# Performance work log

Hardware: AMD Instinct MI355X
Metric: run time of the kernel (lower is better)

Reference implementation:

```python
import jax, jax.numpy as jnp
import numpy as np

N, E, DIN, DH, ED, H, C = 50000, 800000, 384, 256, 32, 4, 64
EPS = 1e-5


def setup_inputs() -> dict:
    key = jax.random.key(0)
    ks = jax.random.split(key, 32)
    w = lambda k, shape, fan: (jax.random.normal(k, shape, jnp.float32) / np.float32(np.sqrt(fan)))
    inp = {
        'x': jax.random.normal(ks[0], (N, DIN), jnp.float32),
        'edge_index': jax.random.randint(ks[1], (2, E), 0, N, dtype=jnp.int32),
        'edge_attr': jax.random.normal(ks[2], (E, ED), jnp.float32),
        'W_in': w(ks[3], (DIN, DH), DIN), 'b_in': jnp.zeros((DH,), jnp.float32),
        'W_out': w(ks[4], (DH, DH), DH), 'b_out': jnp.zeros((DH,), jnp.float32),
    }
    for i in range(2):
        o = 5 + 6 * i
        inp[f'Wl{i}'] = w(ks[o + 0], (DH, H * C), DH)
        inp[f'bl{i}'] = jnp.zeros((H * C,), jnp.float32)
        inp[f'Wr{i}'] = w(ks[o + 1], (DH, H * C), DH)
        inp[f'br{i}'] = jnp.zeros((H * C,), jnp.float32)
        inp[f'We{i}'] = w(ks[o + 2], (ED, H * C), ED)
        inp[f'att{i}'] = w(ks[o + 3], (H, C), C)
        inp[f'bias{i}'] = jnp.zeros((H * C,), jnp.float32)
        inp[f'g{i}'] = jnp.ones((DH,), jnp.float32)
        inp[f'beta{i}'] = jnp.zeros((DH,), jnp.float32)
    return inp


def _gatv2(h, src, dst, ea, Wl, bl, Wr, br, We, att, bias):
    # h: [N, DH]; src/dst: [Etot]; ea: [Etot, ED]
    xl = (h @ Wl + bl).reshape(N, H, C)
    xr = (h @ Wr + br).reshape(N, H, C)
    ee = (ea @ We).reshape(-1, H, C)
    m = jax.nn.leaky_relu(xl[src] + xr[dst] + ee, 0.2)  # [Etot,H,C]
    logits = jnp.einsum('ehc,hc->eh', m, att)           # [Etot,H]
    mx = jax.ops.segment_max(logits, dst, num_segments=N)
    p = jnp.exp(logits - mx[dst])
    den = jax.ops.segment_sum(p, dst, num_segments=N)
    alpha = p / den[dst]                                # softmax per dst node
    out = jax.ops.segment_sum(xl[src] * alpha[:, :, None], dst, num_segments=N)
    return out.reshape(N, H * C) + bias


def _graph_norm(h, g, beta):
    # PyG LayerNorm(mode='graph'), batch=None: normalize over all nodes & channels
    mu = h.mean()
    hc = h - mu
    var = (hc * hc).mean()
    return hc / jnp.sqrt(var + EPS) * g + beta


def reference(x, edge_index, edge_attr, W_in, b_in,
              Wl0, bl0, Wr0, br0, We0, att0, bias0, g0, beta0,
              Wl1, bl1, Wr1, br1, We1, att1, bias1, g1, beta1,
              W_out, b_out):
    loops = jnp.arange(N, dtype=edge_index.dtype)
    src = jnp.concatenate([edge_index[0], loops])
    dst = jnp.concatenate([edge_index[1], loops])
    # self-loop edge_attr filled with mean edge feature (PyG fill_value='mean')
    ea = jnp.concatenate([edge_attr, jnp.broadcast_to(edge_attr.mean(0), (N, ED))], axis=0)
    h = jax.nn.relu(x @ W_in + b_in)
    layers = ((Wl0, bl0, Wr0, br0, We0, att0, bias0, g0, beta0),
              (Wl1, bl1, Wr1, br1, We1, att1, bias1, g1, beta1))
    for Wl, bl, Wr, br, We, att, bias, g, beta in layers:
        hn = jax.nn.elu(_gatv2(h, src, dst, ea, Wl, bl, Wr, br, We, att, bias))
        h = _graph_norm(h + hn, g, beta)
    return h @ W_out + b_out
```

## Files before the change

### kernel.cpp

```cpp
#include <hip/hip_runtime.h>
#include <hip/hip_bf16.h>

#define N_NODES 50000
#define E_EDGES 800000
#define DIN_K   384
#define DH_N    256
#define EPSN    1e-5f

typedef unsigned short ushortT;
typedef __attribute__((ext_vector_type(4))) float f32x4;
typedef __attribute__((ext_vector_type(8))) short bf16x8;

static __device__ __forceinline__ float bf2f(unsigned short u)
{
    return __uint_as_float(((unsigned)u) << 16);
}
static __device__ __forceinline__ unsigned short f2bf(float f)
{
    unsigned u = __float_as_uint(f);
    unsigned r = (u + 0x7fffu + ((u >> 16) & 1u)) >> 16;
    return (unsigned short)r;
}
static __device__ __forceinline__ unsigned pack2(float a, float b)
{
    return (unsigned)f2bf(a) | ((unsigned)f2bf(b) << 16);
}

__global__ __launch_bounds__(256) void ea_accum_kernel(const float* __restrict__ ea,
                                                       float* __restrict__ accum, long total)
{
    long stride = (long)gridDim.x * blockDim.x;
    float local = 0.f;
    for (long i = (long)blockIdx.x * blockDim.x + threadIdx.x; i < total; i += stride)
        local += ea[i];
    __shared__ float red[256];
    red[threadIdx.x] = local;
    __syncthreads();
    if (threadIdx.x < 32) {
        float s = 0.f;
#pragma unroll
        for (int r = 0; r < 8; ++r) s += red[r * 32 + threadIdx.x];
        atomicAdd(&accum[threadIdx.x], s);
    }
}

__global__ void hist_kernel(const int* __restrict__ dst, int* __restrict__ counts, int E)
{
    int stride = gridDim.x * blockDim.x;
    for (int e = blockIdx.x * blockDim.x + threadIdx.x; e < E; e += stride)
        atomicAdd(&counts[dst[e]], 1);
}

__global__ __launch_bounds__(1024) void scan_kernel(const int* __restrict__ counts,
                                                    int* __restrict__ offsets, int Nn)
{
    __shared__ int sdata[1024];
    __shared__ int run_s;
    int tid = threadIdx.x;
    if (tid == 0) run_s = 0;
    __syncthreads();
    for (int base2 = 0; base2 < Nn; base2 += 1024) {
        int i = base2 + tid;
        int v = (i < Nn) ? counts[i] : 0;
        sdata[tid] = v;
        __syncthreads();
        for (int off = 1; off < 1024; off <<= 1) {
            int t = (tid >= off) ? sdata[tid - off] : 0;
            __syncthreads();
            sdata[tid] += t;
            __syncthreads();
        }
        int run = run_s;
        if (i < Nn) offsets[i] = run + sdata[tid] - v;
        int tot = sdata[1023];
        __syncthreads();
        if (tid == 0) run_s = run + tot;
        __syncthreads();
    }
    if (tid == 0) offsets[Nn] = run_s;
}

__global__ void scatter_kernel(const int* __restrict__ src, const int* __restrict__ dst,
                               const int* __restrict__ offsets, int* __restrict__ cursors,
                               int* __restrict__ s_src, int* __restrict__ s_dst,
                               int* __restrict__ s_eid, int E)
{
    int stride = gridDim.x * blockDim.x;
    for (int e = blockIdx.x * blockDim.x + threadIdx.x; e < E; e += stride) {
        int d = dst[e];
        int p = offsets[d] + atomicAdd(&cursors[d], 1);
        s_src[p] = src[e];
        s_dst[p] = d;
        s_eid[p] = e;
    }
}

__global__ void eemean_kernel(const float* __restrict__ accum,
                              const float* __restrict__ We0, const float* __restrict__ We1,
                              float* __restrict__ eemean, float invE)
{
    int tid = threadIdx.x;
    int layer = tid >> 8, c = tid & 255;
    const float* W = layer ? We1 : We0;
    float s = 0.f;
#pragma unroll
    for (int j = 0; j < 32; ++j) s += accum[j] * invE * W[j * 256 + c];
    eemean[layer * 256 + c] = s;
}

__global__ __launch_bounds__(256) void transpose_bf16_kernel(const float* __restrict__ in,
                                                             ushortT* __restrict__ out,
                                                             int K, int N)
{
    __shared__ float tile[32][33];
    int bx = blockIdx.x * 32;
    int by = blockIdx.y * 32;
    int tx = threadIdx.x & 31, ty = threadIdx.x >> 5;
#pragma unroll
    for (int r = 0; r < 32; r += 8) {
        int k = by + ty + r, n = bx + tx;
        if (k < K && n < N) tile[ty + r][tx] = in[(size_t)k * N + n];
    }
    __syncthreads();
#pragma unroll
    for (int r = 0; r < 32; r += 8) {
        int n = bx + ty + r, k = by + tx;
        if (n < N && k < K) out[(size_t)n * K + k] = f2bf(tile[tx][ty + r]);
    }
}

__global__ void fuse_bias_kernel(const float* __restrict__ bl, const float* __restrict__ br,
                                 float* __restrict__ out)
{
    int i = threadIdx.x;
    out[i] = (i < 256) ? bl[i] : br[i - 256];
}

__global__ __launch_bounds__(256) void mfma_gemm_kernel(
    const float* __restrict__ A, const ushortT* __restrict__ Bt,
    const float* __restrict__ bias, float* __restrict__ Cf,
    ushortT* __restrict__ Cb, int K, int Nn, int act)
{
    __shared__ __align__(16) ushortT As[128 * 32];
    __shared__ __align__(16) ushortT Bs[128 * 32];
    int tid = threadIdx.x;
    int brow = blockIdx.x * 128;
    int bcol = blockIdx.y * 128;
    int lane = tid & 63, w = tid >> 6;
    int wr = w >> 1, wc = w & 1;
    int fr = lane & 15, fq = lane >> 4;

    f32x4 acc[4][4];
#pragma unroll
    for (int i = 0; i < 4; ++i)
#pragma unroll
        for (int j = 0; j < 4; ++j)
            acc[i][j] = (f32x4){0.f, 0.f, 0.f, 0.f};

    int r0 = tid >> 2, g0 = tid & 3;
    int r1 = r0 + 64;
    int arow0 = brow + r0, arow1 = brow + r1;
    bool av0 = arow0 < N_NODES, av1 = arow1 < N_NODES;
    const float* Ap0 = A + (size_t)arow0 * K + g0 * 8;
    const float* Ap1 = A + (size_t)arow1 * K + g0 * 8;
    const ushortT* Bp0 = Bt + (size_t)(bcol + r0) * K + g0 * 8;
    const ushortT* Bp1 = Bt + (size_t)(bcol + r1) * K + g0 * 8;
    uint4* asw0 = (uint4*)&As[(size_t)tid * 8];
    uint4* asw1 = (uint4*)&As[(size_t)(tid + 256) * 8];
    uint4* bsw0 = (uint4*)&Bs[(size_t)tid * 8];
    uint4* bsw1 = (uint4*)&Bs[(size_t)(tid + 256) * 8];

    for (int k0 = 0; k0 < K; k0 += 32) {
        float4 z = make_float4(0.f, 0.f, 0.f, 0.f);
        float4 fa0 = z, fa1 = z, fc0 = z, fc1 = z;
        if (av0) { fa0 = *(const float4*)(Ap0 + k0); fc0 = *(const float4*)(Ap0 + k0 + 4); }
        if (av1) { fa1 = *(const float4*)(Ap1 + k0); fc1 = *(const float4*)(Ap1 + k0 + 4); }
        uint4 ub0 = *(const uint4*)(Bp0 + k0);
        uint4 ub1 = *(const uint4*)(Bp1 + k0);
        uint4 ua0, ua1;
        ua0.x = pack2(fa0.x, fa0.y); ua0.y = pack2(fa0.z, fa0.w);
        ua0.z = pack2(fc0.x, fc0.y); ua0.w = pack2(fc0.z, fc0.w);
        ua1.x = pack2(fa1.x, fa1.y); ua1.y = pack2(fa1.z, fa1.w);
        ua1.z = pack2(fc1.x, fc1.y); ua1.w = pack2(fc1.z, fc1.w);
        __syncthreads();
        *asw0 = ua0; *asw1 = ua1;
        *bsw0 = ub0; *bsw1 = ub1;
        __syncthreads();

        bf16x8 af[4], bfv[4];
#pragma unroll
        for (int mi = 0; mi < 4; ++mi)
            af[mi] = *(bf16x8*)&As[(size_t)(wr * 64 + mi * 16 + fr) * 32 + fq * 8];
#pragma unroll
        for (int ni = 0; ni < 4; ++ni)
            bfv[ni] = *(bf16x8*)&Bs[(size_t)(wc * 64 + ni * 16 + fr) * 32 + fq * 8];
#pragma unroll
        for (int mi = 0; mi < 4; ++mi)
#pragma unroll
            for (int ni = 0; ni < 4; ++ni)
                acc[mi][ni] = __builtin_amdgcn_mfma_f32_16x16x32_bf16(
                    af[mi], bfv[ni], acc[mi][ni], 0, 0, 0);
    }

#pragma unroll
    for (int ni = 0; ni < 4; ++ni) {
        int col = bcol + wc * 64 + ni * 16 + fr;
        float bv = bias[col];
#pragma unroll
        for (int mi = 0; mi < 4; ++mi) {
#pragma unroll
            for (int r = 0; r < 4; ++r) {
                int row = brow + wr * 64 + mi * 16 + fq * 4 + r;
                if (row < N_NODES) {
                    float t = acc[mi][ni][r] + bv;
                    if (act == 1) t = t > 0.f ? t : 0.f;
                    if (Cf) Cf[(size_t)row * Nn + col] = t;
                    if (Cb) Cb[(size_t)row * Nn + col] = f2bf(t);
                }
            }
        }
    }
}

__global__ __launch_bounds__(256) void edge_logits_kernel(
    const float* __restrict__ ea, const int* __restrict__ s_eid,
    const int* __restrict__ s_src, const int* __restrict__ s_dst,
    const ushortT* __restrict__ Wet, const float* __restrict__ att,
    const ushortT* __restrict__ xlr, float* __restrict__ logits)
{
    __shared__ __align__(16) ushortT Wet_lds[256 * 40];
    __shared__ float att_lds[256];
    __shared__ int sidx[64], didx[64], eidv[64];
    int tid = threadIdx.x;
    int brow = blockIdx.x * 64;

#pragma unroll
    for (int t = 0; t < 4; ++t) {
        int f = tid + t * 256;
        int row = f >> 2, q = f & 3;
        *(uint4*)&Wet_lds[row * 40 + q * 8] = *(const uint4*)(Wet + (size_t)row * 32 + q * 8);
    }
    att_lds[tid] = att[tid];
    if (tid < 64) {
        sidx[tid] = s_src[brow + tid];
        didx[tid] = s_dst[brow + tid];
        eidv[tid] = s_eid[brow + tid];
    }
    __syncthreads();

    int lane = tid & 63, w = tid >> 6;
    int fr = lane & 15, fq = lane >> 4;
    int e_lane = w * 16 + fr;

    int eid = eidv[e_lane];
    const float* earow = ea + (size_t)eid * 32 + fq * 8;
    float4 f0 = ((const float4*)earow)[0];
    float4 f1 = ((const float4*)earow)[1];
    union { unsigned u[4]; bf16x8 v; } ub;
    ub.u[0] = pack2(f0.x, f0.y);
    ub.u[1] = pack2(f0.z, f0.w);
    ub.u[2] = pack2(f1.x, f1.y);
    ub.u[3] = pack2(f1.z, f1.w);
    bf16x8 bfrag = ub.v;

    f32x4 acc[16];
#pragma unroll
    for (int mi = 0; mi < 16; ++mi) {
        bf16x8 afrag = *(bf16x8*)&Wet_lds[(mi * 16 + fr) * 40 + fq * 8];
        acc[mi] = __builtin_amdgcn_mfma_f32_16x16x32_bf16(
            afrag, bfrag, (f32x4){0.f, 0.f, 0.f, 0.f}, 0, 0, 0);
    }

    int sn = sidx[e_lane], dn = didx[e_lane];
    const ushortT* lxp = xlr + (size_t)sn * 512;
    const ushortT* rxp = xlr + (size_t)dn * 512 + 256;
    float part[4] = {0.f, 0.f, 0.f, 0.f};
#pragma unroll
    for (int mi = 0; mi < 16; ++mi) {
        int ch = mi * 16 + fq * 4;
        ushort4 lx = *(const ushort4*)(lxp + ch);
        ushort4 rx = *(const ushort4*)(rxp + ch);
        float4 at = *(const float4*)&att_lds[ch];
        float t0 = acc[mi][0] + bf2f(lx.x) + bf2f(rx.x); t0 = t0 > 0.f ? t0 : 0.2f * t0;
        float t1 = acc[mi][1] + bf2f(lx.y) + bf2f(rx.y); t1 = t1 > 0.f ? t1 : 0.2f * t1;
        float t2 = acc[mi][2] + bf2f(lx.z) + bf2f(rx.z); t2 = t2 > 0.f ? t2 : 0.2f * t2;
        float t3 = acc[mi][3] + bf2f(lx.w) + bf2f(rx.w); t3 = t3 > 0.f ? t3 : 0.2f * t3;
        part[mi >> 2] += t0 * at.x + t1 * at.y + t2 * at.z + t3 * at.w;
    }
#pragma unroll
    for (int hh = 0; hh < 4; ++hh) {
        part[hh] += __shfl_xor(part[hh], 16);
        part[hh] += __shfl_xor(part[hh], 32);
    }
    if (fq == 0) {
        float4 o = make_float4(part[0], part[1], part[2], part[3]);
        *(float4*)&logits[(size_t)(brow + e_lane) * 4] = o;
    }
}

__global__ __launch_bounds__(256) void edge_attn_kernel(
    const int* __restrict__ s_src, const int* __restrict__ offsets,
    const float* __restrict__ logits,
    const float* __restrict__ att, const float* __restrict__ bias,
    const float* __restrict__ eemean,
    const ushortT* __restrict__ xlr, float* __restrict__ h)
{
    int lane = threadIdx.x & 63;
    int d = blockIdx.x * 4 + (threadIdx.x >> 6);
    size_t xbase = (size_t)d * 512 + lane * 4;
    size_t hbase = (size_t)d * 256 + lane * 4;
    int head = lane >> 4;

    ushort4 xlu = *(const ushort4*)(xlr + xbase);
    ushort4 xru = *(const ushort4*)(xlr + xbase + 256);
    float xr0 = bf2f(xru.x), xr1 = bf2f(xru.y), xr2 = bf2f(xru.z), xr3 = bf2f(xru.w);
    float xs0 = bf2f(xlu.x), xs1 = bf2f(xlu.y), xs2 = bf2f(xlu.z), xs3 = bf2f(xlu.w);
    float4 eem = *(const float4*)(eemean + lane * 4);
    float4 at4 = *(const float4*)(att + lane * 4);

    float m = -1e30f, s = 0.f;
    float acc0 = 0.f, acc1 = 0.f, acc2 = 0.f, acc3 = 0.f;
    int beg = offsets[d], end = offsets[d + 1];

    int idx1 = 0;
    ushort4 x_cur = make_ushort4(0, 0, 0, 0);
    float lg_cur = 0.f;
    if (beg < end) {
        int idx0 = s_src[beg];
        x_cur = *(const ushort4*)(xlr + (size_t)idx0 * 512 + lane * 4);
        lg_cur = logits[(size_t)beg * 4 + head];
        if (beg + 1 < end) idx1 = s_src[beg + 1];
    }

    for (int pos = beg; pos < end; ++pos) {
        ushort4 xv = x_cur;
        float lg = lg_cur;
        int np = pos + 1;
        if (np < end) {
            x_cur = *(const ushort4*)(xlr + (size_t)idx1 * 512 + lane * 4);
            lg_cur = logits[(size_t)np * 4 + head];
        }
        if (pos + 2 < end) idx1 = s_src[pos + 2];

        float nm = fmaxf(m, lg);
        float sc = __expf(m - nm);
        float pr = __expf(lg - nm);
        float v0 = bf2f(xv.x), v1 = bf2f(xv.y), v2 = bf2f(xv.z), v3 = bf2f(xv.w);
        s = s * sc + pr;
        acc0 = acc0 * sc + pr * v0;
        acc1 = acc1 * sc + pr * v1;
        acc2 = acc2 * sc + pr * v2;
        acc3 = acc3 * sc + pr * v3;
        m = nm;
    }

    {
        float t0 = xs0 + xr0 + eem.x; t0 = t0 > 0.f ? t0 : 0.2f * t0;
        float t1 = xs1 + xr1 + eem.y; t1 = t1 > 0.f ? t1 : 0.2f * t1;
        float t2 = xs2 + xr2 + eem.z; t2 = t2 > 0.f ? t2 : 0.2f * t2;
        float t3 = xs3 + xr3 + eem.w; t3 = t3 > 0.f ? t3 : 0.2f * t3;
        float lg = t0 * at4.x + t1 * at4.y + t2 * at4.z + t3 * at4.w;
        lg += __shfl_xor(lg, 1);
        lg += __shfl_xor(lg, 2);
        lg += __shfl_xor(lg, 4);
        lg += __shfl_xor(lg, 8);
        float nm = fmaxf(m, lg);
        float sc = __expf(m - nm);
        float pr = __expf(lg - nm);
        s = s * sc + pr;
        acc0 = acc0 * sc + pr * xs0;
        acc1 = acc1 * sc + pr * xs1;
        acc2 = acc2 * sc + pr * xs2;
        acc3 = acc3 * sc + pr * xs3;
    }

    float inv = 1.f / s;
    float4 b4 = *(const float4*)(bias + lane * 4);
    float4 hv = *(const float4*)(h + hbase);
    float o0 = acc0 * inv + b4.x; o0 = o0 > 0.f ? o0 : __expf(o0) - 1.f;
    float o1 = acc1 * inv + b4.y; o1 = o1 > 0.f ? o1 : __expf(o1) - 1.f;
    float o2 = acc2 * inv + b4.z; o2 = o2 > 0.f ? o2 : __expf(o2) - 1.f;
    float o3 = acc3 * inv + b4.w; o3 = o3 > 0.f ? o3 : __expf(o3) - 1.f;
    *(float4*)(h + hbase) = make_float4(hv.x + o0, hv.y + o1, hv.z + o2, hv.w + o3);
}

__global__ __launch_bounds__(256) void stats_kernel(const float* __restrict__ h,
                                                    float* __restrict__ stats)
{
    int stride = gridDim.x * blockDim.x;
    int total = N_NODES * 64;
    float ls = 0.f, lq = 0.f;
    for (int i = blockIdx.x * blockDim.x + threadIdx.x; i < total; i += stride) {
        float4 v = ((const float4*)h)[i];
        ls += v.x + v.y + v.z + v.w;
        lq += v.x * v.x + v.y * v.y + v.z * v.z + v.w * v.w;
    }
#pragma unroll
    for (int o = 1; o < 64; o <<= 1) {
        ls += __shfl_xor(ls, o);
        lq += __shfl_xor(lq, o);
    }
    __shared__ float red[8];
    int lane = threadIdx.x & 63, w = threadIdx.x >> 6;
    if (lane == 0) { red[w * 2] = ls; red[w * 2 + 1] = lq; }
    __syncthreads();
    if (threadIdx.x == 0) {
        atomicAdd(&stats[0], red[0] + red[2] + red[4] + red[6]);
        atomicAdd(&stats[1], red[1] + red[3] + red[5] + red[7]);
    }
}

__global__ void norm_finalize_kernel(float* __restrict__ stats)
{
    float invM = 1.f / ((float)N_NODES * 256.f);
    float mu = stats[0] * invM;
    float var = stats[1] * invM - mu * mu;
    stats[2] = mu;
    stats[3] = rsqrtf(var + EPSN);
}

__global__ void normalize_kernel(float* __restrict__ h, const float* __restrict__ g,
                                 const float* __restrict__ beta, const float* __restrict__ stats)
{
    float mu = stats[2], sc = stats[3];
    int stride = gridDim.x * blockDim.x;
    int total = N_NODES * 64;
    for (int i = blockIdx.x * blockDim.x + threadIdx.x; i < total; i += stride) {
        float4 v = ((float4*)h)[i];
        int k = (i & 63) * 4;
        float4 gv = *(const float4*)&g[k];
        float4 bv = *(const float4*)&beta[k];
        v.x = (v.x - mu) * sc * gv.x + bv.x;
        v.y = (v.y - mu) * sc * gv.y + bv.y;
        v.z = (v.z - mu) * sc * gv.z + bv.z;
        v.w = (v.w - mu) * sc * gv.w + bv.w;
        ((float4*)h)[i] = v;
    }
}

extern "C" void kernel_launch(void* const* d_in, const int* in_sizes, int n_in,
                              void* d_out, int out_size, void* d_ws, size_t ws_size,
                              hipStream_t stream)
{
    (void)in_sizes; (void)n_in; (void)out_size; (void)ws_size;
    const float* x     = (const float*)d_in[0];
    const int*   eidx  = (const int*)d_in[1];
    const float* ea    = (const float*)d_in[2];
    const float* W_in  = (const float*)d_in[3];
    const float* b_in  = (const float*)d_in[4];
    const float* W_out = (const float*)d_in[5];
    const float* b_out = (const float*)d_in[6];
    const float* Wl[2]  = {(const float*)d_in[7],  (const float*)d_in[16]};
    const float* bl[2]  = {(const float*)d_in[8],  (const float*)d_in[17]};
    const float* Wr[2]  = {(const float*)d_in[9],  (const float*)d_in[18]};
    const float* br[2]  = {(const float*)d_in[10], (const float*)d_in[19]};
    const float* We[2]  = {(const float*)d_in[11], (const float*)d_in[20]};
    const float* att[2] = {(const float*)d_in[12], (const float*)d_in[21]};
    const float* bias[2]= {(const float*)d_in[13], (const float*)d_in[22]};
    const float* g[2]   = {(const float*)d_in[14], (const float*)d_in[23]};
    const float* beta[2]= {(const float*)d_in[15], (const float*)d_in[24]};

    char* p = (char*)d_ws;
    auto take = [&](size_t bytes) -> char* {
        char* r = p;
        p += (bytes + 255) & ~(size_t)255;
        return r;
    };
    int*   counts  = (int*)take((size_t)N_NODES * 4);
    int*   cursors = (int*)take((size_t)N_NODES * 4);
    float* ea_acc  = (float*)take(32 * 4);
    float* stats   = (float*)take(8 * 4);
    size_t zero_bytes = (size_t)(p - (char*)d_ws);
    int*   offsets = (int*)take((size_t)(N_NODES + 1) * 4);
    int*   s_src   = (int*)take((size_t)E_EDGES * 4);
    int*   s_dst   = (int*)take((size_t)E_EDGES * 4);
    int*   s_eid   = (int*)take((size_t)E_EDGES * 4);
    float* eemean  = (float*)take(512 * 4);
    ushortT* WtIn  = (ushortT*)take((size_t)256 * 384 * 2);
    ushortT* WtLR0 = (ushortT*)take((size_t)512 * 256 * 2);
    ushortT* WtLR1 = (ushortT*)take((size_t)512 * 256 * 2);
    ushortT* WtOut = (ushortT*)take((size_t)256 * 256 * 2);
    ushortT* Wet0  = (ushortT*)take((size_t)256 * 32 * 2);
    ushortT* Wet1  = (ushortT*)take((size_t)256 * 32 * 2);
    float* fb0     = (float*)take(512 * 4);
    float* fb1     = (float*)take(512 * 4);
    ushortT* xlr   = (ushortT*)take((size_t)N_NODES * 512 * 2);
    float* h       = (float*)take((size_t)N_NODES * 256 * 4);
    float* logits  = (float*)take((size_t)E_EDGES * 4 * 4);

    const ushortT* WtLR[2] = {WtLR0, WtLR1};
    const ushortT* Wet[2] = {Wet0, Wet1};
    const float* fb[2] = {fb0, fb1};

    const int* srcv = eidx;
    const int* dstv = eidx + E_EDGES;

    hipMemsetAsync(d_ws, 0, zero_bytes, stream);

    ea_accum_kernel<<<512, 256, 0, stream>>>(ea, ea_acc, (long)E_EDGES * 32);
    hist_kernel<<<1024, 256, 0, stream>>>(dstv, counts, E_EDGES);
    scan_kernel<<<1, 1024, 0, stream>>>(counts, offsets, N_NODES);
    scatter_kernel<<<1024, 256, 0, stream>>>(srcv, dstv, offsets, cursors,
                                             s_src, s_dst, s_eid, E_EDGES);
    eemean_kernel<<<1, 512, 0, stream>>>(ea_acc, We[0], We[1], eemean, 1.0f / (float)E_EDGES);

    transpose_bf16_kernel<<<dim3(8, 12), 256, 0, stream>>>(W_in, WtIn, 384, 256);
    transpose_bf16_kernel<<<dim3(8, 8), 256, 0, stream>>>(Wl[0], WtLR0, 256, 256);
    transpose_bf16_kernel<<<dim3(8, 8), 256, 0, stream>>>(Wr[0], WtLR0 + 256 * 256, 256, 256);
    transpose_bf16_kernel<<<dim3(8, 8), 256, 0, stream>>>(Wl[1], WtLR1, 256, 256);
    transpose_bf16_kernel<<<dim3(8, 8), 256, 0, stream>>>(Wr[1], WtLR1 + 256 * 256, 256, 256);
    transpose_bf16_kernel<<<dim3(8, 8), 256, 0, stream>>>(W_out, WtOut, 256, 256);
    transpose_bf16_kernel<<<dim3(8, 1), 256, 0, stream>>>(We[0], Wet0, 32, 256);
    transpose_bf16_kernel<<<dim3(8, 1), 256, 0, stream>>>(We[1], Wet1, 32, 256);
    fuse_bias_kernel<<<1, 512, 0, stream>>>(bl[0], br[0], fb0);
    fuse_bias_kernel<<<1, 512, 0, stream>>>(bl[1], br[1], fb1);

    mfma_gemm_kernel<<<dim3(391, 2), 256, 0, stream>>>(x, WtIn, b_in, h, nullptr, 384, 256, 1);

    for (int l = 0; l < 2; ++l) {
        mfma_gemm_kernel<<<dim3(391, 4), 256, 0, stream>>>(h, WtLR[l], fb[l], nullptr, xlr,
                                                           256, 512, 0);
        edge_logits_kernel<<<E_EDGES / 64, 256, 0, stream>>>(ea, s_eid, s_src, s_dst,
                                                             Wet[l], att[l], xlr, logits);
        edge_attn_kernel<<<N_NODES / 4, 256, 0, stream>>>(s_src, offsets, logits,
                                                          att[l], bias[l], eemean + l * 256,
                                                          xlr, h);
        stats_kernel<<<2048, 256, 0, stream>>>(h, stats + l * 4);
        norm_finalize_kernel<<<1, 1, 0, stream>>>(stats + l * 4);
        normalize_kernel<<<2048, 256, 0, stream>>>(h, g[l], beta[l], stats + l * 4);
    }
    mfma_gemm_kernel<<<dim3(391, 2), 256, 0, stream>>>(h, WtOut, b_out, (float*)d_out, nullptr,
                                                       256, 256, 0);
}
```

Measured before the change: 1.373 ms.

## Fuse setup kernels, fold graph-norm stats into attention, restructure edge logits

Merges the edge-attr mean and dst histogram into one prep kernel, combines the scan with the eemean computation (using a wave-shuffle scan), and folds all weight transposes and bias fusions into one batched launch. The edge-logits kernel now processes 256 edges per block and permutes the Wet rows so that each lane owns a contiguous 64-channel head slice, which allows 16-byte xlr loads and removes the cross-lane shuffle reduction. Graph-norm sum and sum-of-squares are accumulated inside the attention kernel, removing a full pass over h and the finalize launch. Risks include atomic contention on the stats counters from many blocks and higher register pressure in the edge loop.

```diff
diff --git a/kernel.cpp b/kernel.cpp
--- a/kernel.cpp
+++ b/kernel.cpp
@@ -25,13 +25,23 @@
 {
     return (unsigned)f2bf(a) | ((unsigned)f2bf(b) << 16);
 }
-
-__global__ __launch_bounds__(256) void ea_accum_kernel(const float* __restrict__ ea,
-                                                       float* __restrict__ accum, long total)
-{
-    long stride = (long)gridDim.x * blockDim.x;
+static __device__ __forceinline__ void unpack8(uint4 u, float* f)
+{
+    f[0] = bf2f((ushortT)(u.x & 0xffff)); f[1] = bf2f((ushortT)(u.x >> 16));
+    f[2] = bf2f((ushortT)(u.y & 0xffff)); f[3] = bf2f((ushortT)(u.y >> 16));
+    f[4] = bf2f((ushortT)(u.z & 0xffff)); f[5] = bf2f((ushortT)(u.z >> 16));
+    f[6] = bf2f((ushortT)(u.w & 0xffff)); f[7] = bf2f((ushortT)(u.w >> 16));
+}
+
+__global__ __launch_bounds__(256) void prep_kernel(const float* __restrict__ ea,
+                                                   float* __restrict__ accum,
+                                                   const int* __restrict__ dst,
+                                                   int* __restrict__ counts)
+{
+    int gstride = gridDim.x * blockDim.x;
+    long total = (long)E_EDGES * 32;
     float local = 0.f;
-    for (long i = (long)blockIdx.x * blockDim.x + threadIdx.x; i < total; i += stride)
+    for (long i = (long)blockIdx.x * blockDim.x + threadIdx.x; i < total; i += gstride)
         local += ea[i];
     __shared__ float red[256];
     red[threadIdx.x] = local;
@@ -42,42 +52,49 @@
         for (int r = 0; r < 8; ++r) s += red[r * 32 + threadIdx.x];
         atomicAdd(&accum[threadIdx.x], s);
     }
-}
-
-__global__ void hist_kernel(const int* __restrict__ dst, int* __restrict__ counts, int E)
-{
-    int stride = gridDim.x * blockDim.x;
-    for (int e = blockIdx.x * blockDim.x + threadIdx.x; e < E; e += stride)
+    for (int e = blockIdx.x * blockDim.x + threadIdx.x; e < E_EDGES; e += gstride)
         atomicAdd(&counts[dst[e]], 1);
 }
 
-__global__ __launch_bounds__(1024) void scan_kernel(const int* __restrict__ counts,
-                                                    int* __restrict__ offsets, int Nn)
-{
-    __shared__ int sdata[1024];
-    __shared__ int run_s;
-    int tid = threadIdx.x;
-    if (tid == 0) run_s = 0;
-    __syncthreads();
-    for (int base2 = 0; base2 < Nn; base2 += 1024) {
-        int i = base2 + tid;
-        int v = (i < Nn) ? counts[i] : 0;
-        sdata[tid] = v;
+__global__ __launch_bounds__(1024) void scan_eemean_kernel(
+    const int* __restrict__ counts, int* __restrict__ offsets,
+    const float* __restrict__ ea_acc, const float* __restrict__ We0,
+    const float* __restrict__ We1, float* __restrict__ eemean, float invE)
+{
+    __shared__ int wtot[16];
+    int tid = threadIdx.x, lane = tid & 63, wv = tid >> 6;
+    int run = 0;
+    for (int base = 0; base < N_NODES; base += 1024) {
+        int i = base + tid;
+        int v = (i < N_NODES) ? counts[i] : 0;
+        int sc = v;
+#pragma unroll
+        for (int off = 1; off < 64; off <<= 1) {
+            int t = __shfl_up(sc, off);
+            if (lane >= off) sc += t;
+        }
+        if (lane == 63) wtot[wv] = sc;
         __syncthreads();
-        for (int off = 1; off < 1024; off <<= 1) {
-            int t = (tid >= off) ? sdata[tid - off] : 0;
-            __syncthreads();
-            sdata[tid] += t;
-            __syncthreads();
-        }
-        int run = run_s;
-        if (i < Nn) offsets[i] = run + sdata[tid] - v;
-        int tot = sdata[1023];
+        int wpre = 0, tot = 0;
+#pragma unroll
+        for (int k = 0; k < 16; ++k) {
+            int t = wtot[k];
+            if (k < wv) wpre += t;
+            tot += t;
+        }
+        if (i < N_NODES) offsets[i] = run + wpre + sc - v;
+        run += tot;
         __syncthreads();
-        if (tid == 0) run_s = run + tot;
-        __syncthreads();
-    }
-    if (tid == 0) offsets[Nn] = run_s;
+    }
+    if (tid == 0) offsets[N_NODES] = run;
+    if (tid < 512) {
+        int layer = tid >> 8, c = tid & 255;
+        const float* W = layer ? We1 : We0;
+        float s = 0.f;
+#pragma unroll
+        for (int j = 0; j < 32; ++j) s += ea_acc[j] * invE * W[j * 256 + c];
+        eemean[layer * 256 + c] = s;
+    }
 }
 
 __global__ void scatter_kernel(const int* __restrict__ src, const int* __restrict__ dst,
@@ -95,26 +112,43 @@
     }
 }
 
-__global__ void eemean_kernel(const float* __restrict__ accum,
-                              const float* __restrict__ We0, const float* __restrict__ We1,
-                              float* __restrict__ eemean, float invE)
-{
-    int tid = threadIdx.x;
-    int layer = tid >> 8, c = tid & 255;
-    const float* W = layer ? We1 : We0;
-    float s = 0.f;
-#pragma unroll
-    for (int j = 0; j < 32; ++j) s += accum[j] * invE * W[j * 256 + c];
-    eemean[layer * 256 + c] = s;
-}
-
-__global__ __launch_bounds__(256) void transpose_bf16_kernel(const float* __restrict__ in,
-                                                             ushortT* __restrict__ out,
-                                                             int K, int N)
+__global__ __launch_bounds__(256) void transpose_all_kernel(
+    const float* __restrict__ W_in, const float* __restrict__ Wl0,
+    const float* __restrict__ Wr0, const float* __restrict__ Wl1,
+    const float* __restrict__ Wr1, const float* __restrict__ W_out,
+    const float* __restrict__ We0, const float* __restrict__ We1,
+    const float* __restrict__ bl0, const float* __restrict__ br0,
+    const float* __restrict__ bl1, const float* __restrict__ br1,
+    ushortT* __restrict__ WtIn, ushortT* __restrict__ WtLR0,
+    ushortT* __restrict__ WtLR1, ushortT* __restrict__ WtOut,
+    ushortT* __restrict__ Wet0, ushortT* __restrict__ Wet1,
+    float* __restrict__ fb0, float* __restrict__ fb1)
 {
     __shared__ float tile[32][33];
+    int z = blockIdx.z;
+    const float* in; ushortT* out; int K; const int N = 256;
+    switch (z) {
+        case 0: in = W_in;  out = WtIn;            K = 384; break;
+        case 1: in = Wl0;   out = WtLR0;           K = 256; break;
+        case 2: in = Wr0;   out = WtLR0 + 65536;   K = 256; break;
+        case 3: in = Wl1;   out = WtLR1;           K = 256; break;
+        case 4: in = Wr1;   out = WtLR1 + 65536;   K = 256; break;
+        case 5: in = W_out; out = WtOut;           K = 256; break;
+        case 6: in = We0;   out = Wet0;            K = 32;  break;
+        default: in = We1;  out = Wet1;            K = 32;  break;
+    }
+    if (z >= 6 && blockIdx.y == 1) {
+        if (blockIdx.x < 2) {
+            int i = blockIdx.x * 256 + threadIdx.x;
+            float v = (i < 256) ? ((z == 6) ? bl0[i] : bl1[i])
+                                : ((z == 6) ? br0[i - 256] : br1[i - 256]);
+            ((z == 6) ? fb0 : fb1)[i] = v;
+        }
+        return;
+    }
+    int by = blockIdx.y * 32;
+    if (by >= K) return;
     int bx = blockIdx.x * 32;
-    int by = blockIdx.y * 32;
     int tx = threadIdx.x & 31, ty = threadIdx.x >> 5;
 #pragma unroll
     for (int r = 0; r < 32; r += 8) {
@@ -127,13 +161,6 @@
         int n = bx + ty + r, k = by + tx;
         if (n < N && k < K) out[(size_t)n * K + k] = f2bf(tile[tx][ty + r]);
     }
-}
-
-__global__ void fuse_bias_kernel(const float* __restrict__ bl, const float* __restrict__ br,
-                                 float* __restrict__ out)
-{
-    int i = threadIdx.x;
-    out[i] = (i < 256) ? bl[i] : br[i - 256];
 }
 
 __global__ __launch_bounds__(256) void mfma_gemm_kernel(
@@ -230,71 +257,78 @@
 {
     __shared__ __align__(16) ushortT Wet_lds[256 * 40];
     __shared__ float att_lds[256];
-    __shared__ int sidx[64], didx[64], eidv[64];
+    __shared__ int sidx[256], didx[256], eidv[256];
     int tid = threadIdx.x;
-    int brow = blockIdx.x * 64;
+    int brow = blockIdx.x * 256;
 
 #pragma unroll
     for (int t = 0; t < 4; ++t) {
         int f = tid + t * 256;
-        int row = f >> 2, q = f & 3;
-        *(uint4*)&Wet_lds[row * 40 + q * 8] = *(const uint4*)(Wet + (size_t)row * 32 + q * 8);
+        int sr = f >> 2, q = f & 3;
+        int mi = sr >> 4, j = sr & 15;
+        int ch = ((j >> 2) << 6) + mi * 4 + (j & 3);
+        *(uint4*)&Wet_lds[sr * 40 + q * 8] = *(const uint4*)(Wet + (size_t)ch * 32 + q * 8);
     }
     att_lds[tid] = att[tid];
-    if (tid < 64) {
-        sidx[tid] = s_src[brow + tid];
-        didx[tid] = s_dst[brow + tid];
-        eidv[tid] = s_eid[brow + tid];
-    }
+    sidx[tid] = s_src[brow + tid];
+    didx[tid] = s_dst[brow + tid];
+    eidv[tid] = s_eid[brow + tid];
     __syncthreads();
 
     int lane = tid & 63, w = tid >> 6;
     int fr = lane & 15, fq = lane >> 4;
-    int e_lane = w * 16 + fr;
-
-    int eid = eidv[e_lane];
-    const float* earow = ea + (size_t)eid * 32 + fq * 8;
-    float4 f0 = ((const float4*)earow)[0];
-    float4 f1 = ((const float4*)earow)[1];
-    union { unsigned u[4]; bf16x8 v; } ub;
-    ub.u[0] = pack2(f0.x, f0.y);
-    ub.u[1] = pack2(f0.z, f0.w);
-    ub.u[2] = pack2(f1.x, f1.y);
-    ub.u[3] = pack2(f1.z, f1.w);
-    bf16x8 bfrag = ub.v;
-
-    f32x4 acc[16];
-#pragma unroll
-    for (int mi = 0; mi < 16; ++mi) {
-        bf16x8 afrag = *(bf16x8*)&Wet_lds[(mi * 16 + fr) * 40 + fq * 8];
-        acc[mi] = __builtin_amdgcn_mfma_f32_16x16x32_bf16(
-            afrag, bfrag, (f32x4){0.f, 0.f, 0.f, 0.f}, 0, 0, 0);
-    }
-
-    int sn = sidx[e_lane], dn = didx[e_lane];
-    const ushortT* lxp = xlr + (size_t)sn * 512;
-    const ushortT* rxp = xlr + (size_t)dn * 512 + 256;
-    float part[4] = {0.f, 0.f, 0.f, 0.f};
-#pragma unroll
-    for (int mi = 0; mi < 16; ++mi) {
-        int ch = mi * 16 + fq * 4;
-        ushort4 lx = *(const ushort4*)(lxp + ch);
-        ushort4 rx = *(const ushort4*)(rxp + ch);
-        float4 at = *(const float4*)&att_lds[ch];
-        float t0 = acc[mi][0] + bf2f(lx.x) + bf2f(rx.x); t0 = t0 > 0.f ? t0 : 0.2f * t0;
-        float t1 = acc[mi][1] + bf2f(lx.y) + bf2f(rx.y); t1 = t1 > 0.f ? t1 : 0.2f * t1;
-        float t2 = acc[mi][2] + bf2f(lx.z) + bf2f(rx.z); t2 = t2 > 0.f ? t2 : 0.2f * t2;
-        float t3 = acc[mi][3] + bf2f(lx.w) + bf2f(rx.w); t3 = t3 > 0.f ? t3 : 0.2f * t3;
-        part[mi >> 2] += t0 * at.x + t1 * at.y + t2 * at.z + t3 * at.w;
-    }
-#pragma unroll
-    for (int hh = 0; hh < 4; ++hh) {
-        part[hh] += __shfl_xor(part[hh], 16);
-        part[hh] += __shfl_xor(part[hh], 32);
-    }
-    if (fq == 0) {
-        float4 o = make_float4(part[0], part[1], part[2], part[3]);
-        *(float4*)&logits[(size_t)(brow + e_lane) * 4] = o;
+    const float* atp = &att_lds[fq * 64];
+
+#pragma unroll
+    for (int s4 = 0; s4 < 4; ++s4) {
+        int e_lane = w * 64 + s4 * 16 + fr;
+
+        int eid = eidv[e_lane];
+        const float* earow = ea + (size_t)eid * 32 + fq * 8;
+        float4 f0 = ((const float4*)earow)[0];
+        float4 f1 = ((const float4*)earow)[1];
+        union { unsigned u[4]; bf16x8 v; } ub;
+        ub.u[0] = pack2(f0.x, f0.y);
+        ub.u[1] = pack2(f0.z, f0.w);
+        ub.u[2] = pack2(f1.x, f1.y);
+        ub.u[3] = pack2(f1.z, f1.w);
+        bf16x8 bfrag = ub.v;
+
+        f32x4 acc[16];
+#pragma unroll
+        for (int mi = 0; mi < 16; ++mi) {
+            bf16x8 afrag = *(bf16x8*)&Wet_lds[(mi * 16 + fr) * 40 + fq * 8];
+            acc[mi] = __builtin_amdgcn_mfma_f32_16x16x32_bf16(
+                afrag, bfrag, (f32x4){0.f, 0.f, 0.f, 0.f}, 0, 0, 0);
+        }
+
+        int sn = sidx[e_lane], dn = didx[e_lane];
+        const ushortT* lxp = xlr + (size_t)sn * 512 + fq * 64;
+        const ushortT* rxp = xlr + (size_t)dn * 512 + 256 + fq * 64;
+        float lgsum = 0.f;
+#pragma unroll
+        for (int m2 = 0; m2 < 8; ++m2) {
+            uint4 lu = *(const uint4*)(lxp + m2 * 8);
+            uint4 ru = *(const uint4*)(rxp + m2 * 8);
+            float lf[8], rf[8];
+            unpack8(lu, lf);
+            unpack8(ru, rf);
+            float4 a0 = *(const float4*)(atp + m2 * 8);
+            float4 a1 = *(const float4*)(atp + m2 * 8 + 4);
+            f32x4 e0 = acc[2 * m2];
+            f32x4 e1 = acc[2 * m2 + 1];
+            float t0 = e0[0] + lf[0] + rf[0]; t0 = t0 > 0.f ? t0 : 0.2f * t0;
+            float t1 = e0[1] + lf[1] + rf[1]; t1 = t1 > 0.f ? t1 : 0.2f * t1;
+            float t2 = e0[2] + lf[2] + rf[2]; t2 = t2 > 0.f ? t2 : 0.2f * t2;
+            float t3 = e0[3] + lf[3] + rf[3]; t3 = t3 > 0.f ? t3 : 0.2f * t3;
+            float t4 = e1[0] + lf[4] + rf[4]; t4 = t4 > 0.f ? t4 : 0.2f * t4;
+            float t5 = e1[1] + lf[5] + rf[5]; t5 = t5 > 0.f ? t5 : 0.2f * t5;
+            float t6 = e1[2] + lf[6] + rf[6]; t6 = t6 > 0.f ? t6 : 0.2f * t6;
+            float t7 = e1[3] + lf[7] + rf[7]; t7 = t7 > 0.f ? t7 : 0.2f * t7;
+            lgsum += t0 * a0.x + t1 * a0.y + t2 * a0.z + t3 * a0.w
+                   + t4 * a1.x + t5 * a1.y + t6 * a1.z + t7 * a1.w;
+        }
+        logits[(size_t)(brow + e_lane) * 4 + fq] = lgsum;
     }
 }
 
@@ -303,10 +337,12 @@
     const float* __restrict__ logits,
     const float* __restrict__ att, const float* __restrict__ bias,
     const float* __restrict__ eemean,
-    const ushortT* __restrict__ xlr, float* __restrict__ h)
+    const ushortT* __restrict__ xlr, float* __restrict__ h,
+    float* __restrict__ stats)
 {
     int lane = threadIdx.x & 63;
-    int d = blockIdx.x * 4 + (threadIdx.x >> 6);
+    int wv = threadIdx.x >> 6;
+    int d = blockIdx.x * 4 + wv;
     size_t xbase = (size_t)d * 512 + lane * 4;
     size_t hbase = (size_t)d * 256 + lane * 4;
     int head = lane >> 4;
@@ -381,28 +417,18 @@
     float o1 = acc1 * inv + b4.y; o1 = o1 > 0.f ? o1 : __expf(o1) - 1.f;
     float o2 = acc2 * inv + b4.z; o2 = o2 > 0.f ? o2 : __expf(o2) - 1.f;
     float o3 = acc3 * inv + b4.w; o3 = o3 > 0.f ? o3 : __expf(o3) - 1.f;
-    *(float4*)(h + hbase) = make_float4(hv.x + o0, hv.y + o1, hv.z + o2, hv.w + o3);
-}
-
-__global__ __launch_bounds__(256) void stats_kernel(const float* __restrict__ h,
-                                                    float* __restrict__ stats)
-{
-    int stride = gridDim.x * blockDim.x;
-    int total = N_NODES * 64;
-    float ls = 0.f, lq = 0.f;
-    for (int i = blockIdx.x * blockDim.x + threadIdx.x; i < total; i += stride) {
-        float4 v = ((const float4*)h)[i];
-        ls += v.x + v.y + v.z + v.w;
-        lq += v.x * v.x + v.y * v.y + v.z * v.z + v.w * v.w;
-    }
+    float y0 = hv.x + o0, y1 = hv.y + o1, y2 = hv.z + o2, y3 = hv.w + o3;
+    *(float4*)(h + hbase) = make_float4(y0, y1, y2, y3);
+
+    float ls = y0 + y1 + y2 + y3;
+    float lq = y0 * y0 + y1 * y1 + y2 * y2 + y3 * y3;
 #pragma unroll
     for (int o = 1; o < 64; o <<= 1) {
         ls += __shfl_xor(ls, o);
         lq += __shfl_xor(lq, o);
     }
     __shared__ float red[8];
-    int lane = threadIdx.x & 63, w = threadIdx.x >> 6;
-    if (lane == 0) { red[w * 2] = ls; red[w * 2 + 1] = lq; }
+    if (lane == 0) { red[wv * 2] = ls; red[wv * 2 + 1] = lq; }
     __syncthreads();
     if (threadIdx.x == 0) {
         atomicAdd(&stats[0], red[0] + red[2] + red[4] + red[6]);
@@ -410,19 +436,13 @@
     }
 }
 
-__global__ void norm_finalize_kernel(float* __restrict__ stats)
+__global__ void normalize_kernel(float* __restrict__ h, const float* __restrict__ g,
+                                 const float* __restrict__ beta, const float* __restrict__ stats)
 {
     float invM = 1.f / ((float)N_NODES * 256.f);
     float mu = stats[0] * invM;
     float var = stats[1] * invM - mu * mu;
-    stats[2] = mu;
-    stats[3] = rsqrtf(var + EPSN);
-}
-
-__global__ void normalize_kernel(float* __restrict__ h, const float* __restrict__ g,
-                                 const float* __restrict__ beta, const float* __restrict__ stats)
-{
-    float mu = stats[2], sc = stats[3];
+    float sc = rsqrtf(var + EPSN);
     int stride = gridDim.x * blockDim.x;
     int total = N_NODES * 64;
     for (int i = blockIdx.x * blockDim.x + threadIdx.x; i < total; i += stride) {
@@ -497,36 +517,26 @@
 
     hipMemsetAsync(d_ws, 0, zero_bytes, stream);
 
-    ea_accum_kernel<<<512, 256, 0, stream>>>(ea, ea_acc, (long)E_EDGES * 32);
-    hist_kernel<<<1024, 256, 0, stream>>>(dstv, counts, E_EDGES);
-    scan_kernel<<<1, 1024, 0, stream>>>(counts, offsets, N_NODES);
+    prep_kernel<<<1024, 256, 0, stream>>>(ea, ea_acc, dstv, counts);
+    scan_eemean_kernel<<<1, 1024, 0, stream>>>(counts, offsets, ea_acc, We[0], We[1],
+                                               eemean, 1.0f / (float)E_EDGES);
     scatter_kernel<<<1024, 256, 0, stream>>>(srcv, dstv, offsets, cursors,
                                              s_src, s_dst, s_eid, E_EDGES);
-    eemean_kernel<<<1, 512, 0, stream>>>(ea_acc, We[0], We[1], eemean, 1.0f / (float)E_EDGES);
-
-    transpose_bf16_kernel<<<dim3(8, 12), 256, 0, stream>>>(W_in, WtIn, 384, 256);
-    transpose_bf16_kernel<<<dim3(8, 8), 256, 0, stream>>>(Wl[0], WtLR0, 256, 256);
-    transpose_bf16_kernel<<<dim3(8, 8), 256, 0, stream>>>(Wr[0], WtLR0 + 256 * 256, 256, 256);
-    transpose_bf16_kernel<<<dim3(8, 8), 256, 0, stream>>>(Wl[1], WtLR1, 256, 256);
-    transpose_bf16_kernel<<<dim3(8, 8), 256, 0, stream>>>(Wr[1], WtLR1 + 256 * 256, 256, 256);
-    transpose_bf16_kernel<<<dim3(8, 8), 256, 0, stream>>>(W_out, WtOut, 256, 256);
-    transpose_bf16_kernel<<<dim3(8, 1), 256, 0, stream>>>(We[0], Wet0, 32, 256);
-    transpose_bf16_kernel<<<dim3(8, 1), 256, 0, stream>>>(We[1], Wet1, 32, 256);
-    fuse_bias_kernel<<<1, 512, 0, stream>>>(bl[0], br[0], fb0);
-    fuse_bias_kernel<<<1, 512, 0, stream>>>(bl[1], br[1], fb1);
+    transpose_all_kernel<<<dim3(8, 12, 8), 256, 0, stream>>>(
+        W_in, Wl[0], Wr[0], Wl[1], Wr[1], W_out, We[0], We[1],
+        bl[0], br[0], bl[1], br[1],
+        WtIn, WtLR0, WtLR1, WtOut, Wet0, Wet1, fb0, fb1);
 
     mfma_gemm_kernel<<<dim3(391, 2), 256, 0, stream>>>(x, WtIn, b_in, h, nullptr, 384, 256, 1);
 
     for (int l = 0; l < 2; ++l) {
         mfma_gemm_kernel<<<dim3(391, 4), 256, 0, stream>>>(h, WtLR[l], fb[l], nullptr, xlr,
                                                            256, 512, 0);
-        edge_logits_kernel<<<E_EDGES / 64, 256, 0, stream>>>(ea, s_eid, s_src, s_dst,
-                                                             Wet[l], att[l], xlr, logits);
+        edge_logits_kernel<<<E_EDGES / 256, 256, 0, stream>>>(ea, s_eid, s_src, s_dst,
+                                                              Wet[l], att[l], xlr, logits);
         edge_attn_kernel<<<N_NODES / 4, 256, 0, stream>>>(s_src, offsets, logits,
                                                           att[l], bias[l], eemean + l * 256,
-                                                          xlr, h);
-        stats_kernel<<<2048, 256, 0, stream>>>(h, stats + l * 4);
-        norm_finalize_kernel<<<1, 1, 0, stream>>>(stats + l * 4);
+                                                          xlr, h, stats + l * 4);
         normalize_kernel<<<2048, 256, 0, stream>>>(h, g[l], beta[l], stats + l * 4);
     }
     mfma_gemm_kernel<<<dim3(391, 2), 256, 0, stream>>>(h, WtOut, b_out, (float*)d_out, nullptr,
```

New measurement: 1.623 ms. +18.2%, slower.
